# Kernel tuning notes

Measured on AMD Instinct MI355X. Metric: run time of the kernel, lower is better.

## Reference

```python
import jax, jax.numpy as jnp
import numpy as np

N_HEADS = 8
NEG_INF = -1e9


def setup_inputs() -> dict:
    key = jax.random.key(0)
    ks = jax.random.split(key, 9)
    B, S, D = 4, 2048, 512
    scale = 1.0 / np.sqrt(D)
    x = jax.random.normal(ks[0], (B, S, D), dtype=jnp.float32)
    mask = jnp.tril(jnp.ones((S, S), dtype=bool))[None, None, :, :]  # causal [1,1,S,S]
    W_Q_w = jax.random.normal(ks[1], (D, D), dtype=jnp.float32) * scale
    W_Q_b = jax.random.normal(ks[2], (D,), dtype=jnp.float32) * 0.02
    W_K_w = jax.random.normal(ks[3], (D, D), dtype=jnp.float32) * scale
    W_K_b = jax.random.normal(ks[4], (D,), dtype=jnp.float32) * 0.02
    W_V_w = jax.random.normal(ks[5], (D, D), dtype=jnp.float32) * scale
    W_V_b = jax.random.normal(ks[6], (D,), dtype=jnp.float32) * 0.02
    W_O_w = jax.random.normal(ks[7], (D, D), dtype=jnp.float32) * scale
    W_O_b = jax.random.normal(ks[8], (D,), dtype=jnp.float32) * 0.02
    return {"x": x, "mask": mask,
            "W_Q_w": W_Q_w, "W_Q_b": W_Q_b, "W_K_w": W_K_w, "W_K_b": W_K_b,
            "W_V_w": W_V_w, "W_V_b": W_V_b, "W_O_w": W_O_w, "W_O_b": W_O_b}


def reference(x, mask, W_Q_w, W_Q_b, W_K_w, W_K_b, W_V_w, W_V_b, W_O_w, W_O_b):
    B, S, D = x.shape
    H = N_HEADS
    Dh = D // H
    # projections (torch Linear: x @ W.T + b), split heads -> [B,H,S,Dh]
    def split_heads(t):
        return t.reshape(B, S, H, Dh).transpose(0, 2, 1, 3)
    Q = split_heads(x @ W_Q_w.T + W_Q_b)
    K = split_heads(x @ W_K_w.T + W_K_b)
    V = split_heads(x @ W_V_w.T + W_V_b)
    # scaled dot-product attention with explicit [B,H,S,S] scores
    scores = jnp.einsum("bhqd,bhkd->bhqk", Q, K) / jnp.sqrt(jnp.float32(Dh))
    scores = jnp.where(mask, scores, jnp.float32(NEG_INF))
    att = jax.nn.softmax(scores, axis=-1)
    out = jnp.einsum("bhqk,bhkd->bhqd", att, V)
    out = out.transpose(0, 2, 1, 3).reshape(B, S, D)
    return out @ W_O_w.T + W_O_b
```

## Files before the change

kernel.cpp:

```cpp
#include <hip/hip_runtime.h>
#include <hip/hip_bf16.h>

#define BATCH 4
#define SEQ   2048
#define DIM   512
#define NH    8
#define DH    64
#define NTOK  (BATCH*SEQ)

typedef __bf16 bf16x8 __attribute__((ext_vector_type(8)));
typedef float  f32x4  __attribute__((ext_vector_type(4)));

#define MFMA16(a,b,c) __builtin_amdgcn_mfma_f32_16x16x32_bf16((a),(b),(c),0,0,0)

__global__ __launch_bounds__(256) void cvt_f32_bf16(const float* __restrict__ src,
                                                    __bf16* __restrict__ dst, int n8) {
  int i = blockIdx.x * blockDim.x + threadIdx.x;
  if (i >= n8) return;
  const float4* s = (const float4*)src;
  float4 a = s[2*i], b = s[2*i+1];
  bf16x8 o;
  o[0] = (__bf16)a.x; o[1] = (__bf16)a.y; o[2] = (__bf16)a.z; o[3] = (__bf16)a.w;
  o[4] = (__bf16)b.x; o[5] = (__bf16)b.y; o[6] = (__bf16)b.z; o[7] = (__bf16)b.w;
  *(bf16x8*)&dst[8*i] = o;
}

__global__ __launch_bounds__(256) void cvt_weights(
    const float* __restrict__ s0, const float* __restrict__ s1,
    const float* __restrict__ s2, const float* __restrict__ s3,
    __bf16* __restrict__ o0, __bf16* __restrict__ o1,
    __bf16* __restrict__ o2, __bf16* __restrict__ o3) {
  int i = blockIdx.x * blockDim.x + threadIdx.x;
  const int which = i >> 15, off = i & 32767;
  const float* src = (which == 0) ? s0 : (which == 1) ? s1 : (which == 2) ? s2 : s3;
  __bf16* dst      = (which == 0) ? o0 : (which == 1) ? o1 : (which == 2) ? o2 : o3;
  const float4* s = (const float4*)src;
  float4 a = s[2*off], b = s[2*off+1];
  bf16x8 o;
  o[0] = (__bf16)a.x; o[1] = (__bf16)a.y; o[2] = (__bf16)a.z; o[3] = (__bf16)a.w;
  o[4] = (__bf16)b.x; o[5] = (__bf16)b.y; o[6] = (__bf16)b.z; o[7] = (__bf16)b.w;
  *(bf16x8*)&dst[8*off] = o;
}

__global__ __launch_bounds__(256) void gemm_qkv(
    const __bf16* __restrict__ xb,
    const __bf16* __restrict__ wq, const __bf16* __restrict__ wk,
    const __bf16* __restrict__ wv,
    const float* __restrict__ bq, const float* __restrict__ bk,
    const float* __restrict__ bv,
    __bf16* __restrict__ Qb, __bf16* __restrict__ Kb, __bf16* __restrict__ Vt)
{
  const int z = blockIdx.z;
  const __bf16* W    = (z == 0) ? wq : (z == 1) ? wk : wv;
  const float*  bias = (z == 0) ? bq : (z == 1) ? bk : bv;

  __shared__ __bf16 As[128*72];
  __shared__ __bf16 Bs[128*72];

  const int tid  = threadIdx.x;
  const int m0   = blockIdx.x * 128, n0 = blockIdx.y * 128;
  const int w    = tid >> 6, lane = tid & 63, quad = lane >> 4, l16 = lane & 15;
  const int wm   = (w >> 1) * 64, wn = (w & 1) * 64;

  f32x4 acc[4][4] = {};

  for (int k0 = 0; k0 < DIM; k0 += 64) {
#pragma unroll
    for (int i = 0; i < 4; ++i) {
      int c   = tid + i * 256;
      int row = c >> 3;
      int kc  = (c & 7) << 3;
      *(bf16x8*)&As[row*72 + kc] = *(const bf16x8*)&xb[(size_t)(m0+row)*DIM + k0 + kc];
      *(bf16x8*)&Bs[row*72 + kc] = *(const bf16x8*)&W [(size_t)(n0+row)*DIM + k0 + kc];
    }
    __syncthreads();
#pragma unroll
    for (int kk = 0; kk < 2; ++kk) {
      const int ko = kk*32 + quad*8;
      bf16x8 af[4], bfr[4];
#pragma unroll
      for (int f = 0; f < 4; ++f) {
        af[f]  = *(const bf16x8*)&As[(wm + f*16 + l16)*72 + ko];
        bfr[f] = *(const bf16x8*)&Bs[(wn + f*16 + l16)*72 + ko];
      }
#pragma unroll
      for (int fm = 0; fm < 4; ++fm)
#pragma unroll
        for (int fn = 0; fn < 4; ++fn)
          acc[fm][fn] = MFMA16(af[fm], bfr[fn], acc[fm][fn]);
    }
    __syncthreads();
  }

#pragma unroll
  for (int fm = 0; fm < 4; ++fm) {
#pragma unroll
    for (int fn = 0; fn < 4; ++fn) {
      const int col  = n0 + wn + fn*16 + l16;
      const float bc = bias[col];
      const int h = col >> 6, dh = col & 63;
#pragma unroll
      for (int r = 0; r < 4; ++r) {
        const int row = m0 + wm + fm*16 + quad*4 + r;
        const int b = row >> 11, s = row & 2047;
        const float v = acc[fm][fn][r] + bc;
        if (z == 2) {
          Vt[((size_t)(b*NH + h)*DH + dh)*SEQ + s] = (__bf16)v;
        } else {
          __bf16* O = (z == 0) ? Qb : Kb;
          O[((size_t)(b*NH + h)*SEQ + s)*DH + dh] = (__bf16)v;
        }
      }
    }
  }
}

__global__ __launch_bounds__(256) void gemm_out(
    const __bf16* __restrict__ attnb, const __bf16* __restrict__ wo,
    const float* __restrict__ bo, float* __restrict__ out)
{
  __shared__ __bf16 As[128*72];
  __shared__ __bf16 Bs[128*72];

  const int tid = threadIdx.x;
  const int m0  = blockIdx.x * 128, n0 = blockIdx.y * 128;
  const int w   = tid >> 6, lane = tid & 63, quad = lane >> 4, l16 = lane & 15;
  const int wm  = (w >> 1) * 64, wn = (w & 1) * 64;

  f32x4 acc[4][4] = {};

  for (int k0 = 0; k0 < DIM; k0 += 64) {
#pragma unroll
    for (int i = 0; i < 4; ++i) {
      int c   = tid + i * 256;
      int row = c >> 3;
      int kc  = (c & 7) << 3;
      *(bf16x8*)&As[row*72 + kc] = *(const bf16x8*)&attnb[(size_t)(m0+row)*DIM + k0 + kc];
      *(bf16x8*)&Bs[row*72 + kc] = *(const bf16x8*)&wo   [(size_t)(n0+row)*DIM + k0 + kc];
    }
    __syncthreads();
#pragma unroll
    for (int kk = 0; kk < 2; ++kk) {
      const int ko = kk*32 + quad*8;
      bf16x8 af[4], bfr[4];
#pragma unroll
      for (int f = 0; f < 4; ++f) {
        af[f]  = *(const bf16x8*)&As[(wm + f*16 + l16)*72 + ko];
        bfr[f] = *(const bf16x8*)&Bs[(wn + f*16 + l16)*72 + ko];
      }
#pragma unroll
      for (int fm = 0; fm < 4; ++fm)
#pragma unroll
        for (int fn = 0; fn < 4; ++fn)
          acc[fm][fn] = MFMA16(af[fm], bfr[fn], acc[fm][fn]);
    }
    __syncthreads();
  }

#pragma unroll
  for (int fm = 0; fm < 4; ++fm) {
#pragma unroll
    for (int fn = 0; fn < 4; ++fn) {
      const int col  = n0 + wn + fn*16 + l16;
      const float bc = bo[col];
#pragma unroll
      for (int r = 0; r < 4; ++r) {
        const int row = m0 + wm + fm*16 + quad*4 + r;
        out[(size_t)row*DIM + col] = acc[fm][fn][r] + bc;
      }
    }
  }
}

__global__ __launch_bounds__(64) void flash_attn(
    const __bf16* __restrict__ Qb, const __bf16* __restrict__ Kb,
    const __bf16* __restrict__ Vt, __bf16* __restrict__ attnb)
{
  const int idx = blockIdx.x;
  const int bh  = idx & 31;
  const int t   = 63 - (idx >> 5);
  const int b   = bh >> 3, h = bh & 7;
  const int lane = threadIdx.x & 63, quad = lane >> 4, l16 = lane & 15;
  const int q0  = t * 32;

  const __bf16* Qp = Qb + (size_t)bh * SEQ * DH;
  const __bf16* Kp = Kb + (size_t)bh * SEQ * DH;
  const __bf16* Vp = Vt + (size_t)bh * DH * SEQ;

  __shared__ __bf16 Pw[32*72];

  bf16x8 qf[2][2];
#pragma unroll
  for (int mf = 0; mf < 2; ++mf)
#pragma unroll
    for (int kk = 0; kk < 2; ++kk) {
      bf16x8 q = *(const bf16x8*)&Qp[(size_t)(q0 + mf*16 + l16)*DH + kk*32 + quad*8];
#pragma unroll
      for (int j = 0; j < 8; ++j) q[j] = (__bf16)((float)q[j] * 0.125f);
      qf[mf][kk] = q;
    }

  f32x4 of[2][4] = {};
  float m_[2][4], l_[2][4];
#pragma unroll
  for (int mf = 0; mf < 2; ++mf)
#pragma unroll
    for (int r = 0; r < 4; ++r) { m_[mf][r] = -1e30f; l_[mf][r] = 0.f; }

  const int ktiles = (q0 >> 6) + 1;

  bf16x8 kfA[4][2], kfB[4][2];
#pragma unroll
  for (int fn = 0; fn < 4; ++fn)
#pragma unroll
    for (int kk = 0; kk < 2; ++kk)
      kfA[fn][kk] = *(const bf16x8*)&Kp[(size_t)(fn*16 + l16)*DH + kk*32 + quad*8];

#define TILE_STEP(KC, KN, KT)                                                  \
  {                                                                            \
    const int k0 = (KT) * 64;                                                  \
                   \
    bf16x8 vf[4][2];                                                           \
    _Pragma("unroll")                                                          \
    for (int nd = 0; nd < 4; ++nd)                                             \
      _Pragma("unroll")                                                        \
      for (int kq = 0; kq < 2; ++kq)                                           \
        vf[nd][kq] = *(const bf16x8*)&Vp[(size_t)(nd*16 + l16)*SEQ + k0 +      \
                                         kq*32 + quad*8];                      \
                               \
    {                                                                          \
      const int kn0 = ((KT) + 1 < ktiles) ? k0 + 64 : 0;                       \
      _Pragma("unroll")                                                        \
      for (int fn = 0; fn < 4; ++fn)                                           \
        _Pragma("unroll")                                                      \
        for (int kk = 0; kk < 2; ++kk)                                         \
          KN[fn][kk] = *(const bf16x8*)&Kp[(size_t)(kn0 + fn*16 + l16)*DH +    \
                                           kk*32 + quad*8];                    \
    }                                                                          \
                                            \
    f32x4 sf[2][4] = {};                                                       \
    _Pragma("unroll")                                                          \
    for (int mf = 0; mf < 2; ++mf)                                             \
      _Pragma("unroll")                                                        \
      for (int fn = 0; fn < 4; ++fn) {                                         \
        sf[mf][fn] = MFMA16(qf[mf][0], KC[fn][0], sf[mf][fn]);                 \
        sf[mf][fn] = MFMA16(qf[mf][1], KC[fn][1], sf[mf][fn]);                 \
      }                                                                        \
                            \
    if (k0 + 63 > q0) {                                                        \
      _Pragma("unroll")                                                        \
      for (int mf = 0; mf < 2; ++mf)                                           \
        _Pragma("unroll")                                                      \
        for (int fn = 0; fn < 4; ++fn) {                                       \
          const int col = k0 + fn*16 + l16;                                    \
          _Pragma("unroll")                                                    \
          for (int r = 0; r < 4; ++r) {                                        \
            const int row = q0 + mf*16 + quad*4 + r;                           \
            if (col > row) sf[mf][fn][r] = -1e30f;                             \
          }                                                                    \
        }                                                                      \
    }                                                                          \
                                        \
    float rmax[2][4];                                                          \
    _Pragma("unroll")                                                          \
    for (int mf = 0; mf < 2; ++mf)                                             \
      _Pragma("unroll")                                                        \
      for (int r = 0; r < 4; ++r)                                              \
        rmax[mf][r] = fmaxf(fmaxf(sf[mf][0][r], sf[mf][1][r]),                 \
                            fmaxf(sf[mf][2][r], sf[mf][3][r]));                \
    _Pragma("unroll")                                                          \
    for (int d = 1; d < 16; d <<= 1)                                           \
      _Pragma("unroll")                                                        \
      for (int mf = 0; mf < 2; ++mf)                                           \
        _Pragma("unroll")                                                      \
        for (int r = 0; r < 4; ++r)                                            \
          rmax[mf][r] = fmaxf(rmax[mf][r], __shfl_xor(rmax[mf][r], d));        \
    _Pragma("unroll")                                                          \
    for (int mf = 0; mf < 2; ++mf)                                             \
      _Pragma("unroll")                                                        \
      for (int r = 0; r < 4; ++r) {                                            \
        const float mn = fmaxf(m_[mf][r], rmax[mf][r]);                        \
        const float al = __expf(m_[mf][r] - mn);                               \
        m_[mf][r] = mn;                                                        \
        l_[mf][r] *= al;                                                       \
        _Pragma("unroll")                                                      \
        for (int nd = 0; nd < 4; ++nd) of[mf][nd][r] *= al;                    \
      }                                                                        \
    _Pragma("unroll")                                                          \
    for (int mf = 0; mf < 2; ++mf)                                             \
      _Pragma("unroll")                                                        \
      for (int fn = 0; fn < 4; ++fn)                                           \
        _Pragma("unroll")                                                      \
        for (int r = 0; r < 4; ++r)                                            \
          sf[mf][fn][r] = __expf(sf[mf][fn][r] - m_[mf][r]);                   \
    float rsum[2][4];                                                          \
    _Pragma("unroll")                                                          \
    for (int mf = 0; mf < 2; ++mf)                                             \
      _Pragma("unroll")                                                        \
      for (int r = 0; r < 4; ++r)                                              \
        rsum[mf][r] = (sf[mf][0][r] + sf[mf][1][r]) +                          \
                      (sf[mf][2][r] + sf[mf][3][r]);                           \
    _Pragma("unroll")                                                          \
    for (int d = 1; d < 16; d <<= 1)                                           \
      _Pragma("unroll")                                                        \
      for (int mf = 0; mf < 2; ++mf)                                           \
        _Pragma("unroll")                                                      \
        for (int r = 0; r < 4; ++r)                                            \
          rsum[mf][r] += __shfl_xor(rsum[mf][r], d);                           \
    _Pragma("unroll")                                                          \
    for (int mf = 0; mf < 2; ++mf)                                             \
      _Pragma("unroll")                                                        \
      for (int r = 0; r < 4; ++r) l_[mf][r] += rsum[mf][r];                    \
                                           \
    _Pragma("unroll")                                                          \
    for (int mf = 0; mf < 2; ++mf)                                             \
      _Pragma("unroll")                                                        \
      for (int fn = 0; fn < 4; ++fn)                                           \
        _Pragma("unroll")                                                      \
        for (int r = 0; r < 4; ++r)                                            \
          Pw[(mf*16 + quad*4 + r)*72 + fn*16 + l16] = (__bf16)sf[mf][fn][r];   \
    bf16x8 pa[2][2];                                                           \
    _Pragma("unroll")                                                          \
    for (int mf = 0; mf < 2; ++mf)                                             \
      _Pragma("unroll")                                                        \
      for (int kq = 0; kq < 2; ++kq)                                           \
        pa[mf][kq] = *(const bf16x8*)&Pw[(mf*16 + l16)*72 + kq*32 + quad*8];   \
                                                      \
    _Pragma("unroll")                                                          \
    for (int mf = 0; mf < 2; ++mf)                                             \
      _Pragma("unroll")                                                        \
      for (int nd = 0; nd < 4; ++nd) {                                         \
        of[mf][nd] = MFMA16(pa[mf][0], vf[nd][0], of[mf][nd]);                 \
        of[mf][nd] = MFMA16(pa[mf][1], vf[nd][1], of[mf][nd]);                 \
      }                                                                        \
  }

  for (int kt = 0; kt < ktiles; kt += 2) {
    TILE_STEP(kfA, kfB, kt);
    if (kt + 1 < ktiles) TILE_STEP(kfB, kfA, kt + 1);
  }
#undef TILE_STEP

#pragma unroll
  for (int mf = 0; mf < 2; ++mf)
#pragma unroll
    for (int r = 0; r < 4; ++r)
      l_[mf][r] = 1.0f / l_[mf][r];
#pragma unroll
  for (int mf = 0; mf < 2; ++mf)
#pragma unroll
    for (int nd = 0; nd < 4; ++nd) {
      const int dh = nd*16 + l16;
#pragma unroll
      for (int r = 0; r < 4; ++r) {
        const int q = q0 + mf*16 + quad*4 + r;
        attnb[((size_t)b*SEQ + q)*DIM + h*DH + dh] = (__bf16)(of[mf][nd][r] * l_[mf][r]);
      }
    }
}

extern "C" void kernel_launch(void* const* d_in, const int* in_sizes, int n_in,
                              void* d_out, int out_size, void* d_ws, size_t ws_size,
                              hipStream_t stream) {
  const float* x  = (const float*)d_in[0];
  const float* Wq = (const float*)d_in[2];
  const float* bq = (const float*)d_in[3];
  const float* Wk = (const float*)d_in[4];
  const float* bk = (const float*)d_in[5];
  const float* Wv = (const float*)d_in[6];
  const float* bv = (const float*)d_in[7];
  const float* Wo = (const float*)d_in[8];
  const float* bo = (const float*)d_in[9];
  float* out = (float*)d_out;

  __bf16* xb    = (__bf16*)d_ws;
  __bf16* wq    = xb + (size_t)NTOK*DIM;
  __bf16* wk    = wq + DIM*DIM;
  __bf16* wv    = wk + DIM*DIM;
  __bf16* wo    = wv + DIM*DIM;
  __bf16* Qb    = wo + DIM*DIM;
  __bf16* Kb    = Qb + (size_t)NTOK*DIM;
  __bf16* Vt    = Kb + (size_t)NTOK*DIM;
  __bf16* attnb = Vt + (size_t)NTOK*DIM;

  cvt_f32_bf16<<<(NTOK*DIM/8)/256, 256, 0, stream>>>(x, xb, NTOK*DIM/8);
  cvt_weights<<<(4*DIM*DIM/8)/256, 256, 0, stream>>>(Wq, Wk, Wv, Wo, wq, wk, wv, wo);

  gemm_qkv<<<dim3(NTOK/128, DIM/128, 3), 256, 0, stream>>>(
      xb, wq, wk, wv, bq, bk, bv, Qb, Kb, Vt);

  flash_attn<<<2048, 64, 0, stream>>>(Qb, Kb, Vt, attnb);

  gemm_out<<<dim3(NTOK/128, DIM/128), 256, 0, stream>>>(attnb, wo, bo, out);
}
```

Baseline: 210.3 us.

## Split attention KV loop across four waves and stage GEMM tiles via direct global-to-LDS loads

Flash attention now runs four waves per block, each handling a strided subset of key tiles, and their partial softmax states are merged through shared memory at the end. This targets the low occupancy of one-wave blocks and the long serial KV loop for late query tiles. The softmax scale and log2(e) are folded into Q in the QKV GEMM epilogue so the kernel can use exp2. Both GEMMs load tiles with global_load_lds into unpadded 64-wide LDS rows. The cost is an extra LDS merge step and possible LDS bank conflicts from removing the row padding.

```diff
diff --git a/kernel.cpp b/kernel.cpp
--- a/kernel.cpp
+++ b/kernel.cpp
@@ -12,6 +12,20 @@
 typedef float  f32x4  __attribute__((ext_vector_type(4)));
 
 #define MFMA16(a,b,c) __builtin_amdgcn_mfma_f32_16x16x32_bf16((a),(b),(c),0,0,0)
+
+#if __has_builtin(__builtin_amdgcn_exp2f)
+#define EXP2F(x) __builtin_amdgcn_exp2f(x)
+#else
+#define EXP2F(x) exp2f(x)
+#endif
+
+#define QSCALE 0.18033688011112042f
+
+typedef __attribute__((address_space(1))) void GAS;
+typedef __attribute__((address_space(3))) void LAS;
+__device__ __forceinline__ void gl_lds16(const void* g, void* l) {
+  __builtin_amdgcn_global_load_lds((GAS*)g, (LAS*)l, 16, 0, 0);
+}
 
 __global__ __launch_bounds__(256) void cvt_f32_bf16(const float* __restrict__ src,
                                                     __bf16* __restrict__ dst, int n8) {
@@ -54,24 +68,24 @@
   const __bf16* W    = (z == 0) ? wq : (z == 1) ? wk : wv;
   const float*  bias = (z == 0) ? bq : (z == 1) ? bk : bv;
 
-  __shared__ __bf16 As[128*72];
-  __shared__ __bf16 Bs[128*72];
+  __shared__ __align__(16) __bf16 As[128*64];
+  __shared__ __align__(16) __bf16 Bs[128*64];
 
   const int tid  = threadIdx.x;
   const int m0   = blockIdx.x * 128, n0 = blockIdx.y * 128;
   const int w    = tid >> 6, lane = tid & 63, quad = lane >> 4, l16 = lane & 15;
   const int wm   = (w >> 1) * 64, wn = (w & 1) * 64;
+  const int srow = w*32 + (lane >> 3);
+  const int scc  = (lane & 7) * 8;
 
   f32x4 acc[4][4] = {};
 
   for (int k0 = 0; k0 < DIM; k0 += 64) {
 #pragma unroll
     for (int i = 0; i < 4; ++i) {
-      int c   = tid + i * 256;
-      int row = c >> 3;
-      int kc  = (c & 7) << 3;
-      *(bf16x8*)&As[row*72 + kc] = *(const bf16x8*)&xb[(size_t)(m0+row)*DIM + k0 + kc];
-      *(bf16x8*)&Bs[row*72 + kc] = *(const bf16x8*)&W [(size_t)(n0+row)*DIM + k0 + kc];
+      const int row = srow + i*8;
+      gl_lds16(&xb[(size_t)(m0+row)*DIM + k0 + scc], &As[(w*4+i)*512]);
+      gl_lds16(&W [(size_t)(n0+row)*DIM + k0 + scc], &Bs[(w*4+i)*512]);
     }
     __syncthreads();
 #pragma unroll
@@ -80,8 +94,8 @@
       bf16x8 af[4], bfr[4];
 #pragma unroll
       for (int f = 0; f < 4; ++f) {
-        af[f]  = *(const bf16x8*)&As[(wm + f*16 + l16)*72 + ko];
-        bfr[f] = *(const bf16x8*)&Bs[(wn + f*16 + l16)*72 + ko];
+        af[f]  = *(const bf16x8*)&As[(wm + f*16 + l16)*64 + ko];
+        bfr[f] = *(const bf16x8*)&Bs[(wn + f*16 + l16)*64 + ko];
       }
 #pragma unroll
       for (int fm = 0; fm < 4; ++fm)
@@ -106,9 +120,10 @@
         const float v = acc[fm][fn][r] + bc;
         if (z == 2) {
           Vt[((size_t)(b*NH + h)*DH + dh)*SEQ + s] = (__bf16)v;
+        } else if (z == 0) {
+          Qb[((size_t)(b*NH + h)*SEQ + s)*DH + dh] = (__bf16)(v * QSCALE);
         } else {
-          __bf16* O = (z == 0) ? Qb : Kb;
-          O[((size_t)(b*NH + h)*SEQ + s)*DH + dh] = (__bf16)v;
+          Kb[((size_t)(b*NH + h)*SEQ + s)*DH + dh] = (__bf16)v;
         }
       }
     }
@@ -119,24 +134,24 @@
     const __bf16* __restrict__ attnb, const __bf16* __restrict__ wo,
     const float* __restrict__ bo, float* __restrict__ out)
 {
-  __shared__ __bf16 As[128*72];
-  __shared__ __bf16 Bs[128*72];
+  __shared__ __align__(16) __bf16 As[128*64];
+  __shared__ __align__(16) __bf16 Bs[128*64];
 
   const int tid = threadIdx.x;
   const int m0  = blockIdx.x * 128, n0 = blockIdx.y * 128;
   const int w   = tid >> 6, lane = tid & 63, quad = lane >> 4, l16 = lane & 15;
   const int wm  = (w >> 1) * 64, wn = (w & 1) * 64;
+  const int srow = w*32 + (lane >> 3);
+  const int scc  = (lane & 7) * 8;
 
   f32x4 acc[4][4] = {};
 
   for (int k0 = 0; k0 < DIM; k0 += 64) {
 #pragma unroll
     for (int i = 0; i < 4; ++i) {
-      int c   = tid + i * 256;
-      int row = c >> 3;
-      int kc  = (c & 7) << 3;
-      *(bf16x8*)&As[row*72 + kc] = *(const bf16x8*)&attnb[(size_t)(m0+row)*DIM + k0 + kc];
-      *(bf16x8*)&Bs[row*72 + kc] = *(const bf16x8*)&wo   [(size_t)(n0+row)*DIM + k0 + kc];
+      const int row = srow + i*8;
+      gl_lds16(&attnb[(size_t)(m0+row)*DIM + k0 + scc], &As[(w*4+i)*512]);
+      gl_lds16(&wo   [(size_t)(n0+row)*DIM + k0 + scc], &Bs[(w*4+i)*512]);
     }
     __syncthreads();
 #pragma unroll
@@ -145,8 +160,8 @@
       bf16x8 af[4], bfr[4];
 #pragma unroll
       for (int f = 0; f < 4; ++f) {
-        af[f]  = *(const bf16x8*)&As[(wm + f*16 + l16)*72 + ko];
-        bfr[f] = *(const bf16x8*)&Bs[(wn + f*16 + l16)*72 + ko];
+        af[f]  = *(const bf16x8*)&As[(wm + f*16 + l16)*64 + ko];
+        bfr[f] = *(const bf16x8*)&Bs[(wn + f*16 + l16)*64 + ko];
       }
 #pragma unroll
       for (int fm = 0; fm < 4; ++fm)
@@ -172,7 +187,7 @@
   }
 }
 
-__global__ __launch_bounds__(64) void flash_attn(
+__global__ __launch_bounds__(256) void flash_attn(
     const __bf16* __restrict__ Qb, const __bf16* __restrict__ Kb,
     const __bf16* __restrict__ Vt, __bf16* __restrict__ attnb)
 {
@@ -180,25 +195,24 @@
   const int bh  = idx & 31;
   const int t   = 63 - (idx >> 5);
   const int b   = bh >> 3, h = bh & 7;
-  const int lane = threadIdx.x & 63, quad = lane >> 4, l16 = lane & 15;
+  const int tid = threadIdx.x;
+  const int wv  = tid >> 6;
+  const int lane = tid & 63, quad = lane >> 4, l16 = lane & 15;
   const int q0  = t * 32;
 
   const __bf16* Qp = Qb + (size_t)bh * SEQ * DH;
   const __bf16* Kp = Kb + (size_t)bh * SEQ * DH;
   const __bf16* Vp = Vt + (size_t)bh * DH * SEQ;
 
-  __shared__ __bf16 Pw[32*72];
+  __shared__ __align__(16) char smem[3*64*52*4];
+  __bf16* Pw = (__bf16*)(smem + wv*4608);
 
   bf16x8 qf[2][2];
 #pragma unroll
   for (int mf = 0; mf < 2; ++mf)
 #pragma unroll
-    for (int kk = 0; kk < 2; ++kk) {
-      bf16x8 q = *(const bf16x8*)&Qp[(size_t)(q0 + mf*16 + l16)*DH + kk*32 + quad*8];
-#pragma unroll
-      for (int j = 0; j < 8; ++j) q[j] = (__bf16)((float)q[j] * 0.125f);
-      qf[mf][kk] = q;
-    }
+    for (int kk = 0; kk < 2; ++kk)
+      qf[mf][kk] = *(const bf16x8*)&Qp[(size_t)(q0 + mf*16 + l16)*DH + kk*32 + quad*8];
 
   f32x4 of[2][4] = {};
   float m_[2][4], l_[2][4];
@@ -214,7 +228,7 @@
   for (int fn = 0; fn < 4; ++fn)
 #pragma unroll
     for (int kk = 0; kk < 2; ++kk)
-      kfA[fn][kk] = *(const bf16x8*)&Kp[(size_t)(fn*16 + l16)*DH + kk*32 + quad*8];
+      kfA[fn][kk] = *(const bf16x8*)&Kp[(size_t)(wv*64 + fn*16 + l16)*DH + kk*32 + quad*8];
 
 #define TILE_STEP(KC, KN, KT)                                                  \
   {                                                                            \
@@ -227,9 +241,9 @@
       for (int kq = 0; kq < 2; ++kq)                                           \
         vf[nd][kq] = *(const bf16x8*)&Vp[(size_t)(nd*16 + l16)*SEQ + k0 +      \
                                          kq*32 + quad*8];                      \
-                               \
+        \
     {                                                                          \
-      const int kn0 = ((KT) + 1 < ktiles) ? k0 + 64 : 0;                       \
+      const int kn0 = ((KT) + 4 < ktiles) ? k0 + 256 : 0;                      \
       _Pragma("unroll")                                                        \
       for (int fn = 0; fn < 4; ++fn)                                           \
         _Pragma("unroll")                                                      \
@@ -237,7 +251,7 @@
           KN[fn][kk] = *(const bf16x8*)&Kp[(size_t)(kn0 + fn*16 + l16)*DH +    \
                                            kk*32 + quad*8];                    \
     }                                                                          \
-                                            \
+                                   \
     f32x4 sf[2][4] = {};                                                       \
     _Pragma("unroll")                                                          \
     for (int mf = 0; mf < 2; ++mf)                                             \
@@ -246,7 +260,7 @@
         sf[mf][fn] = MFMA16(qf[mf][0], KC[fn][0], sf[mf][fn]);                 \
         sf[mf][fn] = MFMA16(qf[mf][1], KC[fn][1], sf[mf][fn]);                 \
       }                                                                        \
-                            \
+                               \
     if (k0 + 63 > q0) {                                                        \
       _Pragma("unroll")                                                        \
       for (int mf = 0; mf < 2; ++mf)                                           \
@@ -260,7 +274,7 @@
           }                                                                    \
         }                                                                      \
     }                                                                          \
-                                        \
+                           \
     float rmax[2][4];                                                          \
     _Pragma("unroll")                                                          \
     for (int mf = 0; mf < 2; ++mf)                                             \
@@ -280,7 +294,7 @@
       _Pragma("unroll")                                                        \
       for (int r = 0; r < 4; ++r) {                                            \
         const float mn = fmaxf(m_[mf][r], rmax[mf][r]);                        \
-        const float al = __expf(m_[mf][r] - mn);                               \
+        const float al = EXP2F(m_[mf][r] - mn);                                \
         m_[mf][r] = mn;                                                        \
         l_[mf][r] *= al;                                                       \
         _Pragma("unroll")                                                      \
@@ -292,7 +306,7 @@
       for (int fn = 0; fn < 4; ++fn)                                           \
         _Pragma("unroll")                                                      \
         for (int r = 0; r < 4; ++r)                                            \
-          sf[mf][fn][r] = __expf(sf[mf][fn][r] - m_[mf][r]);                   \
+          sf[mf][fn][r] = EXP2F(sf[mf][fn][r] - m_[mf][r]);                    \
     float rsum[2][4];                                                          \
     _Pragma("unroll")                                                          \
     for (int mf = 0; mf < 2; ++mf)                                             \
@@ -311,7 +325,7 @@
     for (int mf = 0; mf < 2; ++mf)                                             \
       _Pragma("unroll")                                                        \
       for (int r = 0; r < 4; ++r) l_[mf][r] += rsum[mf][r];                    \
-                                           \
+              \
     _Pragma("unroll")                                                          \
     for (int mf = 0; mf < 2; ++mf)                                             \
       _Pragma("unroll")                                                        \
@@ -335,28 +349,62 @@
       }                                                                        \
   }
 
-  for (int kt = 0; kt < ktiles; kt += 2) {
+  for (int kt = wv; kt < ktiles; kt += 8) {
     TILE_STEP(kfA, kfB, kt);
-    if (kt + 1 < ktiles) TILE_STEP(kfB, kfA, kt + 1);
+    if (kt + 4 < ktiles) TILE_STEP(kfB, kfA, kt + 4);
   }
 #undef TILE_STEP
 
-#pragma unroll
-  for (int mf = 0; mf < 2; ++mf)
-#pragma unroll
-    for (int r = 0; r < 4; ++r)
-      l_[mf][r] = 1.0f / l_[mf][r];
-#pragma unroll
-  for (int mf = 0; mf < 2; ++mf)
-#pragma unroll
-    for (int nd = 0; nd < 4; ++nd) {
-      const int dh = nd*16 + l16;
-#pragma unroll
-      for (int r = 0; r < 4; ++r) {
-        const int q = q0 + mf*16 + quad*4 + r;
-        attnb[((size_t)b*SEQ + q)*DIM + h*DH + dh] = (__bf16)(of[mf][nd][r] * l_[mf][r]);
+  float* cb = (float*)smem;
+  __syncthreads();
+  if (wv > 0) {
+    float* C = cb + ((wv-1)*64 + lane)*52;
+#pragma unroll
+    for (int mf = 0; mf < 2; ++mf)
+#pragma unroll
+      for (int r = 0; r < 4; ++r) { C[mf*4+r] = m_[mf][r]; C[8+mf*4+r] = l_[mf][r]; }
+#pragma unroll
+    for (int mf = 0; mf < 2; ++mf)
+#pragma unroll
+      for (int nd = 0; nd < 4; ++nd)
+        *(f32x4*)&C[16 + (mf*4+nd)*4] = of[mf][nd];
+  }
+  __syncthreads();
+  if (wv == 0) {
+    for (int wi = 1; wi < 4; ++wi) {
+      const float* C = cb + ((wi-1)*64 + lane)*52;
+#pragma unroll
+      for (int mf = 0; mf < 2; ++mf)
+#pragma unroll
+        for (int r = 0; r < 4; ++r) {
+          const float mo = C[mf*4+r], lo = C[8+mf*4+r];
+          const float mn = fmaxf(m_[mf][r], mo);
+          const float a  = EXP2F(m_[mf][r] - mn);
+          const float bt = EXP2F(mo - mn);
+          m_[mf][r] = mn;
+          l_[mf][r] = l_[mf][r]*a + lo*bt;
+#pragma unroll
+          for (int nd = 0; nd < 4; ++nd)
+            of[mf][nd][r] = of[mf][nd][r]*a + C[16 + (mf*4+nd)*4 + r]*bt;
+        }
+    }
+#pragma unroll
+    for (int mf = 0; mf < 2; ++mf)
+#pragma unroll
+      for (int r = 0; r < 4; ++r)
+        l_[mf][r] = 1.0f / l_[mf][r];
+#pragma unroll
+    for (int mf = 0; mf < 2; ++mf)
+#pragma unroll
+      for (int nd = 0; nd < 4; ++nd) {
+        const int dh = nd*16 + l16;
+#pragma unroll
+        for (int r = 0; r < 4; ++r) {
+          const int q = q0 + mf*16 + quad*4 + r;
+          attnb[((size_t)b*SEQ + q)*DIM + h*DH + dh] = (__bf16)(of[mf][nd][r] * l_[mf][r]);
+        }
       }
-    }
+  }
 }
 
 extern "C" void kernel_launch(void* const* d_in, const int* in_sizes, int n_in,
@@ -389,7 +437,7 @@
   gemm_qkv<<<dim3(NTOK/128, DIM/128, 3), 256, 0, stream>>>(
       xb, wq, wk, wv, bq, bk, bv, Qb, Kb, Vt);
 
-  flash_attn<<<2048, 64, 0, stream>>>(Qb, Kb, Vt, attnb);
+  flash_attn<<<2048, 256, 0, stream>>>(Qb, Kb, Vt, attnb);
 
   gemm_out<<<dim3(NTOK/128, DIM/128), 256, 0, stream>>>(attnb, wo, bo, out);
 }
```

Result: slower. 254.1 us (+20.8%).
